# Performance work log

Measured on AMD Instinct MI355X. Metric: run time of the kernel, lower is better.

The kernel has to match this reference:

```python
import jax, jax.numpy as jnp
import numpy as np

B, S, D, H = 2, 2048, 1024, 16
HD = D // H
MAX_SEQ_LEN = 2048
ROPE_BASE = 10000.0


def _rope(x, pos):
    # x: [B,S,H,HD], pos: [B,S] int positions (already abs+clamped)
    inv_freq = 1.0 / (ROPE_BASE ** (jnp.arange(0, HD, 2, dtype=jnp.float32) / HD))  # [HD/2]
    freqs = pos.astype(jnp.float32)[..., None] * inv_freq  # [B,S,HD/2]
    cos = jnp.cos(freqs)[:, :, None, :]  # [B,S,1,HD/2]
    sin = jnp.sin(freqs)[:, :, None, :]
    x1, x2 = x[..., : HD // 2], x[..., HD // 2 :]
    return jnp.concatenate([x1 * cos - x2 * sin, x2 * cos + x1 * sin], axis=-1)


def setup_inputs() -> dict:
    key = jax.random.key(0)
    ks = jax.random.split(key, 8)
    std = 1.0 / np.sqrt(D)
    x = jax.random.normal(ks[0], (B, S, D), dtype=jnp.float32)
    Wq = jax.random.normal(ks[1], (D, D), dtype=jnp.float32) * std
    Wk = jax.random.normal(ks[2], (D, D), dtype=jnp.float32) * std
    Wv = jax.random.normal(ks[3], (D, D), dtype=jnp.float32) * std
    Wo = jax.random.normal(ks[4], (D, D), dtype=jnp.float32) * std
    bq = jnp.zeros((D,), jnp.float32)
    bk = jnp.zeros((D,), jnp.float32)
    bv = jnp.zeros((D,), jnp.float32)
    bo = jnp.zeros((D,), jnp.float32)
    decay_rate = jnp.float32(0.1)
    # causal mask [B,S,S]
    mask = jnp.broadcast_to(jnp.tril(jnp.ones((S, S), jnp.int32)), (B, S, S))
    # sorted day offsets per batch (monotone time axis)
    days_offset = jnp.sort(jax.random.randint(ks[5], (B, S), 0, MAX_SEQ_LEN), axis=-1).astype(jnp.int32)
    return {"x": x, "Wq": Wq, "bq": bq, "Wk": Wk, "bk": bk, "Wv": Wv, "bv": bv,
            "Wo": Wo, "bo": bo, "decay_rate": decay_rate, "mask": mask, "days_offset": days_offset}


def reference(x, Wq, bq, Wk, bk, Wv, bv, Wo, bo, decay_rate, mask, days_offset):
    b, s, _ = x.shape
    q = (x @ Wq.T + bq).reshape(b, s, H, HD)
    k = (x @ Wk.T + bk).reshape(b, s, H, HD)
    v = (x @ Wv.T + bv).reshape(b, s, H, HD)
    pos = jnp.clip(jnp.abs(days_offset), 0, MAX_SEQ_LEN - 1)
    q = _rope(q, pos)
    k = _rope(k, pos)
    scores = jnp.einsum("bqhd,bkhd->bhqk", q, k) / np.sqrt(HD).astype(np.float32)
    dist = jnp.abs(days_offset[:, :, None] - days_offset[:, None, :]).astype(jnp.float32)  # [B,S,S]
    decay = jnp.exp(-decay_rate * dist)
    scores = scores * decay[:, None, :, :]
    scores = jnp.where(mask[:, None, :, :] == 0, -jnp.inf, scores)
    attn = jax.nn.softmax(scores, axis=-1)
    out = jnp.einsum("bhqk,bkhd->bqhd", attn, v).reshape(b, s, D)
    return out @ Wo.T + bo
```

## Files before the change

kernel.cpp:

```cpp
#include <hip/hip_runtime.h>
#include <hip/hip_bf16.h>


typedef unsigned short u16;
typedef short bf16x8 __attribute__((ext_vector_type(8)));
typedef float f32x4 __attribute__((ext_vector_type(4)));

__device__ __forceinline__ u16 f2bf(float f) {
    unsigned u = __builtin_bit_cast(unsigned, f);
    u += 0x7fffu + ((u >> 16) & 1u);
    return (u16)(u >> 16);
}
__device__ __forceinline__ float bf2f(u16 h) {
    unsigned u = ((unsigned)h) << 16;
    return __builtin_bit_cast(float, u);
}

__global__ __launch_bounds__(256) void convert_all_k(const float* __restrict__ x,
                                                     const float* __restrict__ wq,
                                                     const float* __restrict__ wk,
                                                     const float* __restrict__ wv,
                                                     const float* __restrict__ wo_,
                                                     u16* __restrict__ xb,
                                                     u16* __restrict__ wqkv,
                                                     u16* __restrict__ wob) {
    int i = (blockIdx.x * 256 + threadIdx.x) * 4;
    const float* src;
    u16* dst;
    int off;
    if (i < 4194304) {
        src = x; dst = xb; off = i;
    } else if (i < 5242880) {
        src = wq; dst = wqkv; off = i - 4194304;
    } else if (i < 6291456) {
        src = wk; dst = wqkv + 1048576; off = i - 5242880;
    } else if (i < 7340032) {
        src = wv; dst = wqkv + 2097152; off = i - 6291456;
    } else {
        src = wo_; dst = wob; off = i - 7340032;
    }
    float4 v = *(const float4*)(src + off);
    uint2 o;
    o.x = (unsigned)f2bf(v.x) | ((unsigned)f2bf(v.y) << 16);
    o.y = (unsigned)f2bf(v.z) | ((unsigned)f2bf(v.w) << 16);
    *(uint2*)(dst + off) = o;
}

__global__ __launch_bounds__(256) void gemm_qkv(const u16* __restrict__ A,
                                                const u16* __restrict__ Bw,
                                                const float* __restrict__ bias0,
                                                const float* __restrict__ bias1,
                                                const float* __restrict__ bias2,
                                                const int* __restrict__ days,
                                                u16* __restrict__ outB,
                                                u16* __restrict__ vt,
                                                int M, int N, int K) {
    __shared__ __align__(16) u16 As[2][4096];
    __shared__ __align__(16) u16 Bs[2][4096];
    const int tid = threadIdx.x;
    const int lane = tid & 63;
    const int w = tid >> 6;
    const int wr = w >> 1, wc = w & 1;
    const int lr = lane & 15, lg = lane >> 4;
    const int nbn = N >> 7;
    const int m0 = (blockIdx.x / nbn) << 7;
    const int n0 = (blockIdx.x % nbn) << 7;

    f32x4 acc[4][4] = {};

    const u16* aptr[2];
    const u16* bptr[2];
    int ldsoff[2];
#pragma unroll
    for (int i = 0; i < 2; ++i) {
        int c = (w * 2 + i) * 64 + lane;
        int row = c >> 2, kc = (c & 3) << 3;
        aptr[i] = A + (size_t)(m0 + row) * K + kc;
        bptr[i] = Bw + (size_t)(n0 + row) * K + kc;
        ldsoff[i] = (w * 2 + i) * 512;
    }

#define GSTAGE(K0, BUF)                                                                \
    do {                                                                               \
        _Pragma("unroll") for (int i = 0; i < 2; ++i) {                                \
            __builtin_amdgcn_global_load_lds(                                          \
                (const __attribute__((address_space(1))) void*)(aptr[i] + (K0)),       \
                (__attribute__((address_space(3))) void*)(&As[BUF][ldsoff[i]]), 16, 0, \
                0);                                                                    \
            __builtin_amdgcn_global_load_lds(                                          \
                (const __attribute__((address_space(1))) void*)(bptr[i] + (K0)),       \
                (__attribute__((address_space(3))) void*)(&Bs[BUF][ldsoff[i]]), 16, 0, \
                0);                                                                    \
        }                                                                              \
    } while (0)

    const int nks = K >> 5;
    GSTAGE(0, 0);
    for (int ks = 0; ks < nks; ++ks) {
        const int cur = ks & 1;
        if (ks + 1 < nks) {
            GSTAGE((ks + 1) * 32, cur ^ 1);
            asm volatile("s_waitcnt vmcnt(4)" ::: "memory");
        } else {
            asm volatile("s_waitcnt vmcnt(0)" ::: "memory");
        }
        __builtin_amdgcn_s_barrier();
        bf16x8 af[4], bfr[4];
#pragma unroll
        for (int i = 0; i < 4; ++i)
            af[i] = *(const bf16x8*)(&As[cur][(wr * 64 + i * 16 + lr) * 32 + lg * 8]);
#pragma unroll
        for (int j = 0; j < 4; ++j)
            bfr[j] = *(const bf16x8*)(&Bs[cur][(wc * 64 + j * 16 + lr) * 32 + lg * 8]);
#pragma unroll
        for (int i = 0; i < 4; ++i)
#pragma unroll
            for (int j = 0; j < 4; ++j)
                acc[i][j] = __builtin_amdgcn_mfma_f32_16x16x32_bf16(af[i], bfr[j],
                                                                    acc[i][j], 0, 0, 0);
        __builtin_amdgcn_s_barrier();
    }
#undef GSTAGE

    auto bsel = [&](int ng) -> float {
        return (ng < 1024) ? bias0[ng] : (ng < 2048) ? bias1[ng - 1024] : bias2[ng - 2048];
    };

    if ((n0 + wc * 64) < 2048) {
        const float C1 = -0.41524101186091903f;
        const float inv0 = exp2f((float)lr * C1);
        const float inv1 = exp2f((float)(16 + lr) * C1);
#pragma unroll
        for (int i = 0; i < 4; ++i) {
            int mg = m0 + wr * 64 + i * 16 + lg * 4;
#pragma unroll
            for (int r = 0; r < 4; ++r) {
                int m = mg + r;
                int d = days[m];
                int ad = d < 0 ? -d : d;
                ad = ad > 2047 ? 2047 : ad;
                float pos = (float)ad;
#pragma unroll
                for (int j = 0; j < 2; ++j) {
                    int ng1 = n0 + wc * 64 + j * 16 + lr;
                    int ng2 = ng1 + 32;
                    float x1 = acc[i][j][r] + bsel(ng1);
                    float x2 = acc[i][j + 2][r] + bsel(ng2);
                    float ang = pos * (j ? inv1 : inv0);
                    float sn, cs;
                    __sincosf(ang, &sn, &cs);
                    outB[(size_t)m * 2048 + ng1] = f2bf(x1 * cs - x2 * sn);
                    outB[(size_t)m * 2048 + ng2] = f2bf(x2 * cs + x1 * sn);
                }
            }
        }
    } else {
        const int h = ((n0 + wc * 64) - 2048) >> 6;
#pragma unroll
        for (int i = 0; i < 4; ++i) {
            int mg = m0 + wr * 64 + i * 16 + lg * 4;
            int b = mg >> 11, s0 = mg & 2047;
#pragma unroll
            for (int j = 0; j < 4; ++j) {
                int hd = j * 16 + lr;
                int ng = 2048 + h * 64 + hd;
                float bias = bsel(ng);
                ushort4 o;
                o.x = f2bf(acc[i][j][0] + bias);
                o.y = f2bf(acc[i][j][1] + bias);
                o.z = f2bf(acc[i][j][2] + bias);
                o.w = f2bf(acc[i][j][3] + bias);
                *(ushort4*)&vt[((size_t)(b * 16 + h) * 64 + hd) * 2048 + s0] = o;
            }
        }
    }
}

__global__ __launch_bounds__(512, 2) void gemm_out(const u16* __restrict__ A,
                                                   const u16* __restrict__ Bw,
                                                   const float* __restrict__ bias0,
                                                   float* __restrict__ outF,
                                                   int M, int N, int K) {
    __shared__ __align__(16) u16 As[2][2][4096];
    __shared__ __align__(16) u16 Bs[2][2][4096];
    const int tid = threadIdx.x;
    const int lane = tid & 63;
    const int w4 = (tid >> 6) & 3;
    const int g = tid >> 8;
    const int wr = w4 >> 1, wc = w4 & 1;
    const int lr = lane & 15, lg = lane >> 4;
    const int nbn = N >> 7;
    const int m0 = (blockIdx.x / nbn) << 7;
    const int n0 = (blockIdx.x % nbn) << 7;
    const int kbase = g * (K >> 1);

    f32x4 acc[4][4] = {};

    const u16* aptr[2];
    const u16* bptr[2];
    int ldsoff[2];
#pragma unroll
    for (int i = 0; i < 2; ++i) {
        int c = (w4 * 2 + i) * 64 + lane;
        int row = c >> 2, kc = (c & 3) << 3;
        aptr[i] = A + (size_t)(m0 + row) * K + kbase + kc;
        bptr[i] = Bw + (size_t)(n0 + row) * K + kbase + kc;
        ldsoff[i] = (w4 * 2 + i) * 512;
    }

#define GSTAGE(K0, BUF)                                                                \
    do {                                                                               \
        _Pragma("unroll") for (int i = 0; i < 2; ++i) {                                \
            __builtin_amdgcn_global_load_lds(                                          \
                (const __attribute__((address_space(1))) void*)(aptr[i] + (K0)),       \
                (__attribute__((address_space(3))) void*)(&As[g][BUF][ldsoff[i]]), 16, \
                0, 0);                                                                 \
            __builtin_amdgcn_global_load_lds(                                          \
                (const __attribute__((address_space(1))) void*)(bptr[i] + (K0)),       \
                (__attribute__((address_space(3))) void*)(&Bs[g][BUF][ldsoff[i]]), 16, \
                0, 0);                                                                 \
        }                                                                              \
    } while (0)

    const int nks = K >> 6;
    GSTAGE(0, 0);
    for (int ks = 0; ks < nks; ++ks) {
        const int cur = ks & 1;
        if (ks + 1 < nks) {
            GSTAGE((ks + 1) * 32, cur ^ 1);
            asm volatile("s_waitcnt vmcnt(4)" ::: "memory");
        } else {
            asm volatile("s_waitcnt vmcnt(0)" ::: "memory");
        }
        __builtin_amdgcn_s_barrier();
        bf16x8 af[4], bfr[4];
#pragma unroll
        for (int i = 0; i < 4; ++i)
            af[i] = *(const bf16x8*)(&As[g][cur][(wr * 64 + i * 16 + lr) * 32 + lg * 8]);
#pragma unroll
        for (int j = 0; j < 4; ++j)
            bfr[j] = *(const bf16x8*)(&Bs[g][cur][(wc * 64 + j * 16 + lr) * 32 + lg * 8]);
#pragma unroll
        for (int i = 0; i < 4; ++i)
#pragma unroll
            for (int j = 0; j < 4; ++j)
                acc[i][j] = __builtin_amdgcn_mfma_f32_16x16x32_bf16(af[i], bfr[j],
                                                                    acc[i][j], 0, 0, 0);
        __builtin_amdgcn_s_barrier();
    }
#undef GSTAGE

    float* xch = (float*)&As[0][0][0];
    const int t256 = tid & 255;
#pragma unroll
    for (int hf = 0; hf < 2; ++hf) {
        __syncthreads();
        if (g == 1) {
#pragma unroll
            for (int i = 0; i < 2; ++i)
#pragma unroll
                for (int j = 0; j < 4; ++j)
                    *(f32x4*)&xch[((t256 * 8) + i * 4 + j) * 4] = acc[hf * 2 + i][j];
        }
        __syncthreads();
        if (g == 0) {
#pragma unroll
            for (int i = 0; i < 2; ++i)
#pragma unroll
                for (int j = 0; j < 4; ++j)
                    acc[hf * 2 + i][j] += *(const f32x4*)&xch[((t256 * 8) + i * 4 + j) * 4];
        }
    }
    if (g == 0) {
#pragma unroll
        for (int i = 0; i < 4; ++i) {
            int mg = m0 + wr * 64 + i * 16 + lg * 4;
#pragma unroll
            for (int j = 0; j < 4; ++j) {
                int ng = n0 + wc * 64 + j * 16 + lr;
                float bias = bias0[ng];
#pragma unroll
                for (int r = 0; r < 4; ++r)
                    outF[(size_t)(mg + r) * N + ng] = acc[i][j][r] + bias;
            }
        }
    }
}

__global__ __launch_bounds__(256) void vps_k(const u16* __restrict__ vt,
                                             float* __restrict__ vps) {
    __shared__ float ts[32][32];
    const int bh = blockIdx.x >> 1;
    const int d0 = (blockIdx.x & 1) * 32;
    const int dl = threadIdx.x >> 3;
    const int seg = threadIdx.x & 7;
    const u16* vrow = vt + ((size_t)bh * 64 + d0 + dl) * 2048 + seg * 256;
#pragma unroll
    for (int tt = 0; tt < 4; ++tt) {
        float s = 0.f;
#pragma unroll
        for (int i = 0; i < 8; ++i) {
            bf16x8 v = *(const bf16x8*)(vrow + tt * 64 + i * 8);
#pragma unroll
            for (int e = 0; e < 8; ++e) s += bf2f((u16)v[e]);
        }
        ts[dl][seg * 4 + tt] = s;
    }
    __syncthreads();
    if (threadIdx.x < 32) {
        int d = threadIdx.x;
        float acc = 0.f;
        for (int t = 0; t <= 32; ++t) {
            vps[((size_t)bh * 33 + t) * 64 + d0 + d] = acc;
            if (t < 32) acc += ts[d][t];
        }
    }
}

__device__ __forceinline__ void attn_tile(const u16* __restrict__ Ks,
                                          const u16* __restrict__ Vs,
                                          u16* __restrict__ Pw,
                                          const int* __restrict__ dbk,
                                          float dkmax_c, bf16x8 pconst, float pcr,
                                          bf16x8 bq0, bf16x8 bq1, float dq_c, float c1,
                                          int qrel, bool domask,
                                          float& l_part, f32x4* acc, int lr, int lg) {
    if (!domask && __all(dkmax_c - dq_c < -20.0f)) {
        l_part += 16.0f * pcr;
        __builtin_amdgcn_s_setprio(1);
#pragma unroll
        for (int pv = 0; pv < 2; ++pv) {
            int chunk = pv * 4 + lg;
#pragma unroll
            for (int c = 0; c < 4; ++c) {
                const int r3 = c * 16 + lr;
                bf16x8 bv = *(const bf16x8*)(Vs + r3 * 64 + ((chunk ^ (r3 & 7)) << 3));
                acc[c] = __builtin_amdgcn_mfma_f32_16x16x32_bf16(pconst, bv, acc[c], 0, 0, 0);
            }
        }
        __builtin_amdgcn_s_setprio(0);
        return;
    }
    f32x4 st_acc[4];
    __builtin_amdgcn_s_setprio(1);
#pragma unroll
    for (int st = 0; st < 4; ++st) {
        const int r2 = st * 16 + lr;
        const u16* kr = Ks + r2 * 64;
        bf16x8 ka0 = *(const bf16x8*)(kr + ((lg ^ (r2 & 7)) << 3));
        bf16x8 ka1 = *(const bf16x8*)(kr + (((4 + lg) ^ (r2 & 7)) << 3));
        f32x4 t = {};
        t = __builtin_amdgcn_mfma_f32_16x16x32_bf16(ka0, bq0, t, 0, 0, 0);
        t = __builtin_amdgcn_mfma_f32_16x16x32_bf16(ka1, bq1, t, 0, 0, 0);
        st_acc[st] = t;
    }
    __builtin_amdgcn_s_setprio(0);
    const float L2E = 1.4426950408889634f;
    const float POFF = 17.312340490667562f;
    float p[4][4];
#pragma unroll
    for (int st = 0; st < 4; ++st) {
        int4 dk4 = *(const int4*)(dbk + st * 16 + lg * 4);
#pragma unroll
        for (int r = 0; r < 4; ++r) {
            float dkf = (float)((&dk4.x)[r]);
            float dec = exp2f(__builtin_fmaf(dkf, c1, -dq_c));
            float v = st_acc[st][r] * dec;
            p[st][r] = exp2f(__builtin_fmaf(v, L2E, -POFF));
        }
    }
    if (domask) {
#pragma unroll
        for (int st = 0; st < 4; ++st)
#pragma unroll
            for (int r = 0; r < 4; ++r)
                p[st][r] = (st * 16 + lg * 4 + r <= qrel) ? p[st][r] : 0.f;
    }
#pragma unroll
    for (int st = 0; st < 4; ++st)
#pragma unroll
        for (int r = 0; r < 4; ++r) l_part += p[st][r];
#pragma unroll
    for (int st = 0; st < 4; ++st) {
        unsigned lo, hi;
        asm("v_cvt_pk_bf16_f32 %0, %1, %2" : "=v"(lo) : "v"(p[st][0]), "v"(p[st][1]));
        asm("v_cvt_pk_bf16_f32 %0, %1, %2" : "=v"(hi) : "v"(p[st][2]), "v"(p[st][3]));
        uint2 pk;
        pk.x = lo;
        pk.y = hi;
        int chunk = st * 2 + (lg >> 1);
        int idx = lr * 64 + ((chunk ^ (lr & 7)) << 3) + ((lg & 1) << 2);
        *(uint2*)&Pw[idx] = pk;
    }
    __builtin_amdgcn_s_setprio(1);
#pragma unroll
    for (int pv = 0; pv < 2; ++pv) {
        int chunk = pv * 4 + lg;
        bf16x8 pa = *(const bf16x8*)&Pw[lr * 64 + ((chunk ^ (lr & 7)) << 3)];
#pragma unroll
        for (int c = 0; c < 4; ++c) {
            const int r3 = c * 16 + lr;
            bf16x8 bv = *(const bf16x8*)(Vs + r3 * 64 + ((chunk ^ (r3 & 7)) << 3));
            acc[c] = __builtin_amdgcn_mfma_f32_16x16x32_bf16(pa, bv, acc[c], 0, 0, 0);
        }
    }
    __builtin_amdgcn_s_setprio(0);
}

__global__ __launch_bounds__(256, 4) void attn_k(const u16* __restrict__ qkv,
                                                 const u16* __restrict__ vt,
                                                 const int* __restrict__ days,
                                                 const float* __restrict__ decay_p,
                                                 const float* __restrict__ vps,
                                                 u16* __restrict__ attn_out) {
    __shared__ __align__(16) u16 Ks[2][4096];
    __shared__ __align__(16) u16 Vs[2][4096];
    __shared__ __align__(16) u16 Plds[4][1024];
    const int tid = threadIdx.x;
    const int lane = tid & 63;
    const int w = tid >> 6;
    const int lr = lane & 15, lg = lane >> 4;
    const int wg = (blockIdx.x & 7) * 128 + (blockIdx.x >> 3);
    const int qt = wg & 31;
    const int bh = wg >> 5;
    const int b = bh >> 4, h = bh & 15;
    const int qb = qt * 64 + w * 16;
    const float rate = decay_p[0];
    const float c1 = rate * 1.4426950408889634f;

    const u16* qmat = qkv + (size_t)b * 2048 * 2048 + h * 64;
    const u16* kmat = qmat + 1024;
    const u16* vtm = vt + (size_t)bh * 64 * 2048;
    const int* db = days + b * 2048;

    const int cp0 = (w * 2 + 0) * 64 + lane;
    const int cp1 = (w * 2 + 1) * 64 + lane;
    const int r0 = cp0 >> 3, c0 = cp0 & 7;
    const int r1 = cp1 >> 3, c1i = cp1 & 7;
    const u16* ksrc0 = kmat + (size_t)r0 * 2048 + ((c0 ^ (r0 & 7)) << 3);
    const u16* ksrc1 = kmat + (size_t)r1 * 2048 + ((c1i ^ (r1 & 7)) << 3);
    const u16* vsrc0 = vtm + (size_t)r0 * 2048 + ((c0 ^ (r0 & 7)) << 3);
    const u16* vsrc1 = vtm + (size_t)r1 * 2048 + ((c1i ^ (r1 & 7)) << 3);
    const int doff0 = (w * 2 + 0) * 512;
    const int doff1 = (w * 2 + 1) * 512;

#define STAGE(T, SLOT)                                                                 \
    do {                                                                               \
        __builtin_amdgcn_global_load_lds(                                              \
            (const __attribute__((address_space(1))) void*)(ksrc0 +                    \
                                                            (size_t)(T) * 64 * 2048), \
            (__attribute__((address_space(3))) void*)(&Ks[SLOT][doff0]), 16, 0, 0);    \
        __builtin_amdgcn_global_load_lds(                                              \
            (const __attribute__((address_space(1))) void*)(ksrc1 +                    \
                                                            (size_t)(T) * 64 * 2048), \
            (__attribute__((address_space(3))) void*)(&Ks[SLOT][doff1]), 16, 0, 0);    \
        __builtin_amdgcn_global_load_lds(                                              \
            (const __attribute__((address_space(1))) void*)(vsrc0 + (size_t)(T) * 64), \
            (__attribute__((address_space(3))) void*)(&Vs[SLOT][doff0]), 16, 0, 0);    \
        __builtin_amdgcn_global_load_lds(                                              \
            (const __attribute__((address_space(1))) void*)(vsrc1 + (size_t)(T) * 64), \
            (__attribute__((address_space(3))) void*)(&Vs[SLOT][doff1]), 16, 0, 0);    \
    } while (0)

    const float dq00_c = (float)db[qt * 64] * c1 + 3.0f;
    int t0;
    {
        const int l32 = lane & 31;
        float dm = (float)db[l32 * 64 + 63] * c1;
        bool cnd = (lane < qt) && (dm < dq00_c - 20.0f);
        unsigned long long m = __ballot(cnd);
        t0 = (int)__builtin_ctzll(~m);
    }

    STAGE(t0, 0);

    bf16x8 bq0, bq1;
    {
        const u16* qp = qmat + (size_t)(qb + lr) * 2048 + lg * 8;
        bq0 = *(const bf16x8*)qp;
        bq1 = *(const bf16x8*)(qp + 32);
    }
    const float dq_c = (float)db[qb + lr] * c1 + 3.0f;

    const u16 pcu = f2bf(exp2f(-17.312340490667562f));
    const float pcr = bf2f(pcu);
    bf16x8 pconst;
#pragma unroll
    for (int i = 0; i < 8; ++i) pconst[i] = (short)pcu;

    float lp = (float)t0 * 16.0f * pcr;
    f32x4 acc[4];
#pragma unroll
    for (int c = 0; c < 4; ++c) {
        float vv = pcr * vps[((size_t)bh * 33 + t0) * 64 + c * 16 + lr];
        acc[c] = (f32x4){vv, vv, vv, vv};
    }

    for (int kt = t0; kt <= qt; ++kt) {
        const int cur = (kt - t0) & 1;
        if (kt < qt) {
            STAGE(kt + 1, cur ^ 1);
            asm volatile("s_waitcnt vmcnt(4)" ::: "memory");
        } else {
            asm volatile("s_waitcnt vmcnt(0)" ::: "memory");
        }
        __builtin_amdgcn_s_barrier();
        const int* dbk = db + kt * 64;
        const float dkmax_c = (float)dbk[63] * c1;
        attn_tile(Ks[cur], Vs[cur], Plds[w], dbk, dkmax_c, pconst, pcr,
                  bq0, bq1, dq_c, c1, w * 16 + lr, kt == qt, lp, acc, lr, lg);
        __builtin_amdgcn_s_barrier();
    }
#undef STAGE

    float l_full = lp + __shfl_xor(lp, 16);
    l_full += __shfl_xor(l_full, 32);
    float inv_[4];
#pragma unroll
    for (int r = 0; r < 4; ++r) inv_[r] = 1.0f / __shfl(l_full, lg * 4 + r);
#pragma unroll
    for (int c = 0; c < 4; ++c)
#pragma unroll
        for (int r = 0; r < 4; ++r) {
            const int qg = qb + lg * 4 + r;
            attn_out[(size_t)(b * 2048 + qg) * 1024 + h * 64 + c * 16 + lr] =
                f2bf(acc[c][r] * inv_[r]);
        }
}

extern "C" void kernel_launch(void* const* d_in, const int* in_sizes, int n_in,
                              void* d_out, int out_size, void* d_ws, size_t ws_size,
                              hipStream_t stream) {
    const float* x = (const float*)d_in[0];
    const float* Wq = (const float*)d_in[1];
    const float* bq = (const float*)d_in[2];
    const float* Wk = (const float*)d_in[3];
    const float* bk = (const float*)d_in[4];
    const float* Wv = (const float*)d_in[5];
    const float* bv = (const float*)d_in[6];
    const float* Wo = (const float*)d_in[7];
    const float* bo = (const float*)d_in[8];
    const float* decay = (const float*)d_in[9];
    const int* days = (const int*)d_in[11];
    float* out = (float*)d_out;

    char* ws = (char*)d_ws;
    u16* xb = (u16*)(ws);
    u16* wqkv = (u16*)(ws + 8388608);
    u16* wo = (u16*)(ws + 14680064);
    u16* qkb = (u16*)(ws + 16777216);
    u16* vtb = (u16*)(ws + 41943040);
    u16* attb = (u16*)(ws + 50331648);
    float* vpsb = (float*)(ws + 58720256);

    convert_all_k<<<8192, 256, 0, stream>>>(x, Wq, Wk, Wv, Wo, xb, wqkv, wo);

    gemm_qkv<<<768, 256, 0, stream>>>(xb, wqkv, bq, bk, bv, days, qkb, vtb, 4096,
                                      3072, 1024);
    vps_k<<<64, 256, 0, stream>>>(vtb, vpsb);
    attn_k<<<1024, 256, 0, stream>>>(qkb, vtb, days, decay, vpsb, attb);
    gemm_out<<<256, 512, 0, stream>>>(attb, wo, bo, out, 4096, 1024, 1024);
}
```

Baseline: 101.5 us.

## Enlarge QKV GEMM tile to 256x128 with 512 threads and XCD-aware block remap

Switches the QKV projection GEMM to 512-thread blocks that each compute a 256x128 output tile, so every B-weight tile loaded into LDS is reused across twice as many rows. It also remaps block IDs so consecutive blocks are spread across the 8 XCDs, which is meant to improve L2 locality. The load-staging counts and vmcnt wait are adjusted to match. In the attention kernel, the day-offset pointer is now computed directly from the days input instead of a local variable. The larger tile uses more LDS and produces fewer blocks, which may hurt occupancy or tail balance.

Measured after the change: 219.0 us. +115.9%, slower.

```diff
diff --git a/kernel.cpp b/kernel.cpp
--- a/kernel.cpp
+++ b/kernel.cpp
@@ -46,16 +46,16 @@
     *(uint2*)(dst + off) = o;
 }
 
-__global__ __launch_bounds__(256) void gemm_qkv(const u16* __restrict__ A,
-                                                const u16* __restrict__ Bw,
-                                                const float* __restrict__ bias0,
-                                                const float* __restrict__ bias1,
-                                                const float* __restrict__ bias2,
-                                                const int* __restrict__ days,
-                                                u16* __restrict__ outB,
-                                                u16* __restrict__ vt,
-                                                int M, int N, int K) {
-    __shared__ __align__(16) u16 As[2][4096];
+__global__ __launch_bounds__(512, 6) void gemm_qkv(const u16* __restrict__ A,
+                                                   const u16* __restrict__ Bw,
+                                                   const float* __restrict__ bias0,
+                                                   const float* __restrict__ bias1,
+                                                   const float* __restrict__ bias2,
+                                                   const int* __restrict__ days,
+                                                   u16* __restrict__ outB,
+                                                   u16* __restrict__ vt,
+                                                   int M, int N, int K) {
+    __shared__ __align__(16) u16 As[2][8192];
     __shared__ __align__(16) u16 Bs[2][4096];
     const int tid = threadIdx.x;
     const int lane = tid & 63;
@@ -63,21 +63,28 @@
     const int wr = w >> 1, wc = w & 1;
     const int lr = lane & 15, lg = lane >> 4;
     const int nbn = N >> 7;
-    const int m0 = (blockIdx.x / nbn) << 7;
-    const int n0 = (blockIdx.x % nbn) << 7;
+    const int wgid = (blockIdx.x & 7) * 48 + (blockIdx.x >> 3);
+    const int m0 = (wgid / nbn) << 8;
+    const int n0 = (wgid % nbn) << 7;
 
     f32x4 acc[4][4] = {};
 
     const u16* aptr[2];
-    const u16* bptr[2];
-    int ldsoff[2];
+    int aoff[2];
 #pragma unroll
     for (int i = 0; i < 2; ++i) {
-        int c = (w * 2 + i) * 64 + lane;
+        int c = w * 128 + i * 64 + lane;
         int row = c >> 2, kc = (c & 3) << 3;
         aptr[i] = A + (size_t)(m0 + row) * K + kc;
-        bptr[i] = Bw + (size_t)(n0 + row) * K + kc;
-        ldsoff[i] = (w * 2 + i) * 512;
+        aoff[i] = (w * 128 + i * 64) * 8;
+    }
+    const u16* bptr;
+    int boff;
+    {
+        int c = w * 64 + lane;
+        int row = c >> 2, kc = (c & 3) << 3;
+        bptr = Bw + (size_t)(n0 + row) * K + kc;
+        boff = (w * 64) * 8;
     }
 
 #define GSTAGE(K0, BUF)                                                                \
@@ -85,13 +92,12 @@
         _Pragma("unroll") for (int i = 0; i < 2; ++i) {                                \
             __builtin_amdgcn_global_load_lds(                                          \
                 (const __attribute__((address_space(1))) void*)(aptr[i] + (K0)),       \
-                (__attribute__((address_space(3))) void*)(&As[BUF][ldsoff[i]]), 16, 0, \
-                0);                                                                    \
-            __builtin_amdgcn_global_load_lds(                                          \
-                (const __attribute__((address_space(1))) void*)(bptr[i] + (K0)),       \
-                (__attribute__((address_space(3))) void*)(&Bs[BUF][ldsoff[i]]), 16, 0, \
+                (__attribute__((address_space(3))) void*)(&As[BUF][aoff[i]]), 16, 0,   \
                 0);                                                                    \
         }                                                                              \
+        __builtin_amdgcn_global_load_lds(                                              \
+            (const __attribute__((address_space(1))) void*)(bptr + (K0)),              \
+            (__attribute__((address_space(3))) void*)(&Bs[BUF][boff]), 16, 0, 0);      \
     } while (0)
 
     const int nks = K >> 5;
@@ -100,7 +106,7 @@
         const int cur = ks & 1;
         if (ks + 1 < nks) {
             GSTAGE((ks + 1) * 32, cur ^ 1);
-            asm volatile("s_waitcnt vmcnt(4)" ::: "memory");
+            asm volatile("s_waitcnt vmcnt(3)" ::: "memory");
         } else {
             asm volatile("s_waitcnt vmcnt(0)" ::: "memory");
         }
@@ -505,7 +511,7 @@
             asm volatile("s_waitcnt vmcnt(0)" ::: "memory");
         }
         __builtin_amdgcn_s_barrier();
-        const int* dbk = db + kt * 64;
+        const int* dbk = days + b * 2048 + kt * 64;
         const float dkmax_c = (float)dbk[63] * c1;
         attn_tile(Ks[cur], Vs[cur], Plds[w], dbk, dkmax_c, pconst, pcr,
                   bq0, bq1, dq_c, c1, w * 16 + lr, kt == qt, lp, acc, lr, lg);
@@ -555,7 +561,7 @@
 
     convert_all_k<<<8192, 256, 0, stream>>>(x, Wq, Wk, Wv, Wo, xb, wqkv, wo);
 
-    gemm_qkv<<<768, 256, 0, stream>>>(xb, wqkv, bq, bk, bv, days, qkb, vtb, 4096,
+    gemm_qkv<<<384, 512, 0, stream>>>(xb, wqkv, bq, bk, bv, days, qkb, vtb, 4096,
                                       3072, 1024);
     vps_k<<<64, 256, 0, stream>>>(vtb, vpsb);
     attn_k<<<1024, 256, 0, stream>>>(qkb, vtb, days, decay, vpsb, attb);
```
